# Kernel optimization log

Measured on AMD Instinct MI355X. Metric: run time of the kernel, lower is better.

Reference implementation:

```python
import jax, jax.numpy as jnp
import numpy as np

N_NODES = 100000
N_EDGES = 1600000
IN_CH = 50


def setup_inputs() -> dict:
    key = jax.random.key(0)
    ks = jax.random.split(key, 6)
    x = jax.random.normal(ks[0], (N_NODES, IN_CH), dtype=jnp.float32)
    edge_index = jax.random.randint(ks[1], (2, N_EDGES), 0, N_NODES, dtype=jnp.int32)
    # Glorot-ish scaled weights
    W1 = jax.random.normal(ks[2], (2 * IN_CH, 64), dtype=jnp.float32) * (1.0 / np.sqrt(2 * IN_CH))
    b1 = jnp.zeros((64,), jnp.float32)
    W2 = jax.random.normal(ks[3], (2 * 64, 32), dtype=jnp.float32) * (1.0 / np.sqrt(2 * 64))
    b2 = jnp.zeros((32,), jnp.float32)
    W3 = jax.random.normal(ks[4], (32, 1), dtype=jnp.float32) * (1.0 / np.sqrt(32))
    b3 = jnp.zeros((1,), jnp.float32)
    return {"x": x, "edge_index": edge_index, "W1": W1, "b1": b1,
            "W2": W2, "b2": b2, "W3": W3, "b3": b3}


def _sage_conv(x, src, dst, W, b, n_nodes):
    # mean aggregation of neighbor (source) features onto target nodes
    msg = x[src]                                             # [E, d] gather
    agg = jax.ops.segment_sum(msg, dst, num_segments=n_nodes)  # [N, d]
    cnt = jax.ops.segment_sum(jnp.ones(src.shape[0], x.dtype), dst,
                              num_segments=n_nodes)            # [N]
    mean = agg / jnp.maximum(cnt, 1.0)[:, None]
    h = jnp.concatenate([x, mean], axis=-1)                  # concat=True
    return h @ W + b


def reference(x, edge_index, W1, b1, W2, b2, W3, b3):
    src, dst = edge_index[0], edge_index[1]
    n = x.shape[0]
    h = jax.nn.relu(_sage_conv(x, src, dst, W1, b1, n))
    h = jax.nn.relu(_sage_conv(h, src, dst, W2, b2, n))
    return h @ W3 + b3  # [N, 1]
```

## Files before the change

kernel.cpp:

```cpp
#include <hip/hip_runtime.h>
#include <hip/hip_bf16.h>

#define N_NODES 100000
#define N_EDGES 1600000
#define IN_CH 50
#define NPB 256
#define NB ((N_NODES + NPB - 1) / NPB)
#define CAPLOG 13
#define EPB 4096
#define NBLK_A ((N_EDGES + EPB - 1) / EPB)
#define PAD_BLOCKS ((N_NODES * 64) / 1024)

__global__ __launch_bounds__(1024) void bin_pad_kernel(
    const int* __restrict__ src, const int* __restrict__ dst,
    int* __restrict__ cursor_rel, unsigned* __restrict__ binned,
    const float* __restrict__ x, unsigned short* __restrict__ xb) {
    if (blockIdx.x >= NBLK_A) {
        int t = (blockIdx.x - NBLK_A) * 1024 + threadIdx.x;
        int n = t >> 6, c = t & 63;
        float v = (c < IN_CH) ? x[n * IN_CH + c] : 0.0f;
        __hip_bfloat16 hb = __float2bfloat16(v);
        xb[t] = *(unsigned short*)&hb;
        return;
    }
    __shared__ int bc[NB];
    __shared__ int boff[NB];
    int t = threadIdx.x;
    if (t < NB) bc[t] = 0;
    __syncthreads();
    int e0 = blockIdx.x * EPB;
    int e1 = min(e0 + EPB, N_EDGES);
    for (int i = e0 + t; i < e1; i += 1024)
        atomicAdd(&bc[dst[i] >> 8], 1);
    __syncthreads();
    if (t < NB) {
        int v = bc[t];
        int rel = v ? atomicAdd(&cursor_rel[t], v) : 0;
        boff[t] = (t << CAPLOG) + rel;
        bc[t] = 0;
    }
    __syncthreads();
    for (int i = e0 + t; i < e1; i += 1024) {
        int d = dst[i];
        int b = d >> 8;
        int k = atomicAdd(&bc[b], 1);
        binned[boff[b] + k] = ((unsigned)(d & 255) << 17) | (unsigned)src[i];
    }
}

__global__ __launch_bounds__(1024) void bucket_fine(
    const unsigned* __restrict__ binned, const int* __restrict__ cursor_rel,
    int* __restrict__ cnt, int* __restrict__ row_start, int* __restrict__ csr_src) {
    __shared__ int lcnt[NPB];
    __shared__ int lofs[NPB];
    __shared__ int sc[NPB];
    int t = threadIdx.x;
    int b = blockIdx.x;
    int nbase = b * NPB;
    int bbase = b << CAPLOG;
    int ecnt  = cursor_rel[b];
    if (t < NPB) lcnt[t] = 0;
    __syncthreads();
    for (int i = t; i < ecnt; i += 1024)
        atomicAdd(&lcnt[(binned[bbase + i] >> 17) & 255], 1);
    __syncthreads();
    int v = (t < NPB) ? lcnt[t] : 0;
    if (t < NPB) sc[t] = v;
    __syncthreads();
    for (int off = 1; off < NPB; off <<= 1) {
        int tmp = (t < NPB && t >= off) ? sc[t - off] : 0;
        __syncthreads();
        if (t < NPB) sc[t] += tmp;
        __syncthreads();
    }
    if (t < NPB) {
        int excl = sc[t] - v;
        lofs[t] = excl;
        int n = nbase + t;
        if (n < N_NODES) { cnt[n] = v; row_start[n] = bbase + excl; }
    }
    __syncthreads();
    for (int i = t; i < ecnt; i += 1024) {
        unsigned p = binned[bbase + i];
        int d = (int)((p >> 17) & 255);
        int k = atomicAdd(&lofs[d], 1);
        csr_src[bbase + k] = (int)(p & 0x1FFFFu);
    }
}

__device__ __forceinline__ void upadd8(float* a, uint4 v, float p) {
    a[0] = fmaf(p, __uint_as_float(v.x << 16), a[0]);
    a[1] = fmaf(p, __uint_as_float(v.x & 0xffff0000u), a[1]);
    a[2] = fmaf(p, __uint_as_float(v.y << 16), a[2]);
    a[3] = fmaf(p, __uint_as_float(v.y & 0xffff0000u), a[3]);
    a[4] = fmaf(p, __uint_as_float(v.z << 16), a[4]);
    a[5] = fmaf(p, __uint_as_float(v.z & 0xffff0000u), a[5]);
    a[6] = fmaf(p, __uint_as_float(v.w << 16), a[6]);
    a[7] = fmaf(p, __uint_as_float(v.w & 0xffff0000u), a[7]);
}

#define WAVE_LDS_FENCE() __asm__ volatile("s_waitcnt lgkmcnt(0)" ::: "memory")

__device__ __forceinline__ void gather2(
    const unsigned short* __restrict__ featb, const int* __restrict__ csr_src,
    const int* __restrict__ row_start, const int* __restrict__ cnt,
    int nb, int lane, float acc[2][8]) {
    int g  = lane >> 3;
    int cw = (lane & 7) * 8;
    int start[2], deg[2], sv[2];
    #pragma unroll
    for (int i = 0; i < 2; ++i) {
        start[i] = row_start[nb + i];
        deg[i]   = cnt[nb + i];
        #pragma unroll
        for (int c = 0; c < 8; ++c) acc[i][c] = 0.f;
    }
    int dmax = max(deg[0], deg[1]);
    #pragma unroll
    for (int i = 0; i < 2; ++i)
        sv[i] = (lane < deg[i]) ? csr_src[start[i] + lane] : 0;

    #pragma unroll
    for (int cb = 0; cb < 64; cb += 16) {
        if (cb >= dmax) break;
        int s00 = __shfl(sv[0], cb + g);
        int s01 = __shfl(sv[0], cb + 8 + g);
        int s10 = __shfl(sv[1], cb + g);
        int s11 = __shfl(sv[1], cb + 8 + g);
        uint4 v00 = *(const uint4*)(featb + s00 * 64 + cw);
        uint4 v01 = *(const uint4*)(featb + s01 * 64 + cw);
        uint4 v10 = *(const uint4*)(featb + s10 * 64 + cw);
        uint4 v11 = *(const uint4*)(featb + s11 * 64 + cw);
        int rem0 = deg[0] - cb;
        int rem1 = deg[1] - cb;
        upadd8(acc[0], v00, (g < rem0) ? 1.f : 0.f);
        upadd8(acc[0], v01, (g + 8 < rem0) ? 1.f : 0.f);
        upadd8(acc[1], v10, (g < rem1) ? 1.f : 0.f);
        upadd8(acc[1], v11, (g + 8 < rem1) ? 1.f : 0.f);
    }
    if (dmax > 64) {
        for (int i = 0; i < 2; ++i) {
            for (int c0 = 64; c0 < deg[i]; c0 += 64) {
                int rem = deg[i] - c0; if (rem > 64) rem = 64;
                int sx = (lane < rem) ? csr_src[start[i] + c0 + lane] : 0;
                for (int cb = 0; cb < rem; cb += 16) {
                    int s0 = __shfl(sx, cb + g);
                    int s1 = __shfl(sx, cb + 8 + g);
                    float p0 = (cb + g < rem) ? 1.f : 0.f;
                    float p1 = (cb + 8 + g < rem) ? 1.f : 0.f;
                    uint4 v0 = *(const uint4*)(featb + s0 * 64 + cw);
                    uint4 v1 = *(const uint4*)(featb + s1 * 64 + cw);
                    upadd8(acc[i], v0, p0);
                    upadd8(acc[i], v1, p1);
                }
            }
        }
    }
    #pragma unroll
    for (int i = 0; i < 2; ++i) {
        float inv = 1.0f / fmaxf((float)deg[i], 1.0f);
        #pragma unroll
        for (int c = 0; c < 8; ++c) {
            float t = acc[i][c];
            t += __shfl_xor(t, 8);
            t += __shfl_xor(t, 16);
            t += __shfl_xor(t, 32);
            acc[i][c] = t * inv;
        }
    }
}

__device__ __forceinline__ float bf16u(unsigned short u) {
    return __uint_as_float(((unsigned)u) << 16);
}

__global__ __launch_bounds__(256, 8) void layer1_fused(
    const unsigned short* __restrict__ xb,
    const int* __restrict__ csr_src, const int* __restrict__ row_start,
    const int* __restrict__ cnt, const float* __restrict__ W1,
    const float* __restrict__ b1, unsigned short* __restrict__ h1b) {
    int wv   = threadIdx.x >> 6;
    int lane = threadIdx.x & 63;
    int nb   = (blockIdx.x * 4 + wv) * 2;

    float acc[2][8];
    gather2(xb, csr_src, row_start, cnt, nb, lane, acc);

    __shared__ __align__(16) float selfF[4][2][64];
    __shared__ __align__(16) float meanF[4][2][64];
    #pragma unroll
    for (int i = 0; i < 2; ++i) {
        selfF[wv][i][lane] = bf16u(xb[((nb + i) << 6) + lane]);
        if (lane < 8) {
            *(float4*)&meanF[wv][i][lane * 8] =
                make_float4(acc[i][0], acc[i][1], acc[i][2], acc[i][3]);
            *(float4*)&meanF[wv][i][lane * 8 + 4] =
                make_float4(acc[i][4], acc[i][5], acc[i][6], acc[i][7]);
        }
    }
    WAVE_LDS_FENCE();

    float ao[2];
    float bb = b1[lane];
    #pragma unroll
    for (int i = 0; i < 2; ++i) ao[i] = bb;
    #pragma unroll
    for (int k = 0; k < IN_CH; ++k) {
        float w = W1[k * 64 + lane];
        #pragma unroll
        for (int i = 0; i < 2; ++i) ao[i] = fmaf(selfF[wv][i][k], w, ao[i]);
    }
    #pragma unroll
    for (int k = 0; k < IN_CH; ++k) {
        float w = W1[(IN_CH + k) * 64 + lane];
        #pragma unroll
        for (int i = 0; i < 2; ++i) ao[i] = fmaf(meanF[wv][i][k], w, ao[i]);
    }
    #pragma unroll
    for (int i = 0; i < 2; ++i) {
        float r = fmaxf(ao[i], 0.f);
        __hip_bfloat16 hb = __float2bfloat16(r);
        h1b[((nb + i) << 6) + lane] = *(unsigned short*)&hb;
    }
}

__global__ __launch_bounds__(256, 8) void layer23_fused(
    const unsigned short* __restrict__ h1b,
    const int* __restrict__ csr_src, const int* __restrict__ row_start,
    const int* __restrict__ cnt, const float* __restrict__ W2,
    const float* __restrict__ b2, const float* __restrict__ W3,
    const float* __restrict__ b3, float* __restrict__ out) {
    int wv   = threadIdx.x >> 6;
    int lane = threadIdx.x & 63;
    int nb   = (blockIdx.x * 4 + wv) * 2;

    float acc[2][8];
    gather2(h1b, csr_src, row_start, cnt, nb, lane, acc);

    __shared__ __align__(16) float featL[4][2][128];
    #pragma unroll
    for (int i = 0; i < 2; ++i) {
        featL[wv][i][lane] = bf16u(h1b[((nb + i) << 6) + lane]);
        if (lane < 8) {
            *(float4*)&featL[wv][i][64 + lane * 8] =
                make_float4(acc[i][0], acc[i][1], acc[i][2], acc[i][3]);
            *(float4*)&featL[wv][i][64 + lane * 8 + 4] =
                make_float4(acc[i][4], acc[i][5], acc[i][6], acc[i][7]);
        }
    }
    WAVE_LDS_FENCE();

    int hh = lane >> 5;
    int j  = lane & 31;
    float a0 = b2[j];
    #pragma unroll
    for (int k = 0; k < 128; ++k) {
        float w = W2[k * 32 + j];
        a0 = fmaf(featL[wv][hh][k], w, a0);
    }
    float w3 = W3[j];
    float c3 = b3[0];
    float v0 = fmaxf(a0, 0.f) * w3;
    #pragma unroll
    for (int off = 1; off <= 16; off <<= 1)
        v0 += __shfl_xor(v0, off);
    if (j == 0)
        out[nb + hh] = v0 + c3;
}

extern "C" void kernel_launch(void* const* d_in, const int* in_sizes, int n_in,
                              void* d_out, int out_size, void* d_ws, size_t ws_size,
                              hipStream_t stream) {
    const float* x   = (const float*)d_in[0];
    const int*   ei  = (const int*)d_in[1];
    const int*   src = ei;
    const int*   dst = ei + N_EDGES;
    const float* W1  = (const float*)d_in[2];
    const float* b1  = (const float*)d_in[3];
    const float* W2  = (const float*)d_in[4];
    const float* b2  = (const float*)d_in[5];
    const float* W3  = (const float*)d_in[6];
    const float* b3  = (const float*)d_in[7];
    float* out = (float*)d_out;

    char* ws = (char*)d_ws;
    auto align = [](size_t v) { return (v + 255) & ~(size_t)255; };
    size_t o = 0;
    int* cursor_rel = (int*)(ws + o); o = align(o + 512 * 4);
    int* cnt       = (int*)(ws + o); o = align(o + (size_t)N_NODES * 4);
    int* row_start = (int*)(ws + o); o = align(o + (size_t)N_NODES * 4);
    unsigned* binned = (unsigned*)(ws + o); o = align(o + ((size_t)NB << CAPLOG) * 4);
    int* csr_src   = (int*)(ws + o); o = align(o + ((size_t)NB << CAPLOG) * 4);
    unsigned short* xb  = (unsigned short*)(ws + o); o = align(o + (size_t)N_NODES * 64 * 2);
    unsigned short* h1b = (unsigned short*)(ws + o); o = align(o + (size_t)N_NODES * 64 * 2);

    (void)hipMemsetAsync(cursor_rel, 0, 512 * sizeof(int), stream);

    bin_pad_kernel<<<NBLK_A + PAD_BLOCKS, 1024, 0, stream>>>(src, dst, cursor_rel,
                                                             binned, x, xb);
    bucket_fine<<<NB, 1024, 0, stream>>>(binned, cursor_rel, cnt, row_start, csr_src);

    layer1_fused<<<N_NODES / 8, 256, 0, stream>>>(xb, csr_src, row_start, cnt,
                                                  W1, b1, h1b);
    layer23_fused<<<N_NODES / 8, 256, 0, stream>>>(h1b, csr_src, row_start, cnt,
                                                   W2, b2, W3, b3, out);
}
```

Baseline: 249.6 us.

## Apply layer-2 weight before aggregation to halve gathered feature width

Because mean aggregation is linear, layer 1 now also multiplies h1 by both halves of W2, storing the self-projection in fp32 and the neighbor-projection in bf16 (32 channels). Layer 2 then gathers 32-wide bf16 rows instead of 64-wide, so the random-access edge gather moves half the bytes, and it only adds the two terms before ReLU and W3. The price is extra FMA work and a new fp32 intermediate in layer 1, plus a different bf16 rounding point for the aggregated values.

Result: slower. 418.9 us (+67.8%).

```diff
diff --git a/kernel.cpp b/kernel.cpp
--- a/kernel.cpp
+++ b/kernel.cpp
@@ -178,7 +178,9 @@
     const unsigned short* __restrict__ xb,
     const int* __restrict__ csr_src, const int* __restrict__ row_start,
     const int* __restrict__ cnt, const float* __restrict__ W1,
-    const float* __restrict__ b1, unsigned short* __restrict__ h1b) {
+    const float* __restrict__ b1, const float* __restrict__ W2,
+    const float* __restrict__ b2,
+    unsigned short* __restrict__ y2b, float* __restrict__ yselff) {
     int wv   = threadIdx.x >> 6;
     int lane = threadIdx.x & 63;
     int nb   = (blockIdx.x * 4 + wv) * 2;
@@ -216,35 +218,111 @@
         #pragma unroll
         for (int i = 0; i < 2; ++i) ao[i] = fmaf(meanF[wv][i][k], w, ao[i]);
     }
-    #pragma unroll
-    for (int i = 0; i < 2; ++i) {
-        float r = fmaxf(ao[i], 0.f);
-        __hip_bfloat16 hb = __float2bfloat16(r);
-        h1b[((nb + i) << 6) + lane] = *(unsigned short*)&hb;
-    }
+
+    __shared__ __align__(16) float h1F[4][2][64];
+    #pragma unroll
+    for (int i = 0; i < 2; ++i)
+        h1F[wv][i][lane] = fmaxf(ao[i], 0.f);
+    WAVE_LDS_FENCE();
+
+    int hh = lane >> 5;
+    int j  = lane & 31;
+    float ys = b2[j];
+    float ym = 0.f;
+    #pragma unroll
+    for (int k = 0; k < 64; ++k) {
+        float h = h1F[wv][hh][k];
+        ys = fmaf(h, W2[k * 32 + j], ys);
+        ym = fmaf(h, W2[(64 + k) * 32 + j], ym);
+    }
+    yselff[(nb + hh) * 32 + j] = ys;
+    __hip_bfloat16 hb = __float2bfloat16(ym);
+    y2b[(nb + hh) * 32 + j] = *(unsigned short*)&hb;
 }
 
 __global__ __launch_bounds__(256, 8) void layer23_fused(
-    const unsigned short* __restrict__ h1b,
+    const unsigned short* __restrict__ y2b,
     const int* __restrict__ csr_src, const int* __restrict__ row_start,
-    const int* __restrict__ cnt, const float* __restrict__ W2,
-    const float* __restrict__ b2, const float* __restrict__ W3,
-    const float* __restrict__ b3, float* __restrict__ out) {
+    const int* __restrict__ cnt, const float* __restrict__ yselff,
+    const float* __restrict__ W3, const float* __restrict__ b3,
+    float* __restrict__ out) {
     int wv   = threadIdx.x >> 6;
     int lane = threadIdx.x & 63;
     int nb   = (blockIdx.x * 4 + wv) * 2;
-
+    int g  = lane >> 2;
+    int cw = (lane & 3) * 8;
+
+    int start[2], deg[2], sv[2];
     float acc[2][8];
-    gather2(h1b, csr_src, row_start, cnt, nb, lane, acc);
-
-    __shared__ __align__(16) float featL[4][2][128];
-    #pragma unroll
-    for (int i = 0; i < 2; ++i) {
-        featL[wv][i][lane] = bf16u(h1b[((nb + i) << 6) + lane]);
-        if (lane < 8) {
-            *(float4*)&featL[wv][i][64 + lane * 8] =
+    #pragma unroll
+    for (int i = 0; i < 2; ++i) {
+        start[i] = row_start[nb + i];
+        deg[i]   = cnt[nb + i];
+        #pragma unroll
+        for (int c = 0; c < 8; ++c) acc[i][c] = 0.f;
+    }
+    int dmax = max(deg[0], deg[1]);
+    #pragma unroll
+    for (int i = 0; i < 2; ++i)
+        sv[i] = (lane < deg[i]) ? csr_src[start[i] + lane] : 0;
+
+    #pragma unroll
+    for (int cb = 0; cb < 64; cb += 32) {
+        if (cb >= dmax) break;
+        int s00 = __shfl(sv[0], cb + g);
+        int s01 = __shfl(sv[0], cb + 16 + g);
+        int s10 = __shfl(sv[1], cb + g);
+        int s11 = __shfl(sv[1], cb + 16 + g);
+        uint4 v00 = *(const uint4*)(y2b + s00 * 32 + cw);
+        uint4 v01 = *(const uint4*)(y2b + s01 * 32 + cw);
+        uint4 v10 = *(const uint4*)(y2b + s10 * 32 + cw);
+        uint4 v11 = *(const uint4*)(y2b + s11 * 32 + cw);
+        int rem0 = deg[0] - cb;
+        int rem1 = deg[1] - cb;
+        upadd8(acc[0], v00, (g < rem0) ? 1.f : 0.f);
+        upadd8(acc[0], v01, (g + 16 < rem0) ? 1.f : 0.f);
+        upadd8(acc[1], v10, (g < rem1) ? 1.f : 0.f);
+        upadd8(acc[1], v11, (g + 16 < rem1) ? 1.f : 0.f);
+    }
+    if (dmax > 64) {
+        for (int i = 0; i < 2; ++i) {
+            for (int c0 = 64; c0 < deg[i]; c0 += 64) {
+                int rem = deg[i] - c0; if (rem > 64) rem = 64;
+                int sx = (lane < rem) ? csr_src[start[i] + c0 + lane] : 0;
+                for (int cb = 0; cb < rem; cb += 32) {
+                    int s0 = __shfl(sx, cb + g);
+                    int s1 = __shfl(sx, cb + 16 + g);
+                    float p0 = (cb + g < rem) ? 1.f : 0.f;
+                    float p1 = (cb + 16 + g < rem) ? 1.f : 0.f;
+                    uint4 v0 = *(const uint4*)(y2b + s0 * 32 + cw);
+                    uint4 v1 = *(const uint4*)(y2b + s1 * 32 + cw);
+                    upadd8(acc[i], v0, p0);
+                    upadd8(acc[i], v1, p1);
+                }
+            }
+        }
+    }
+
+    __shared__ __align__(16) float aggF[4][2][32];
+    #pragma unroll
+    for (int i = 0; i < 2; ++i) {
+        float inv = 1.0f / fmaxf((float)deg[i], 1.0f);
+        #pragma unroll
+        for (int c = 0; c < 8; ++c) {
+            float t = acc[i][c];
+            t += __shfl_xor(t, 4);
+            t += __shfl_xor(t, 8);
+            t += __shfl_xor(t, 16);
+            t += __shfl_xor(t, 32);
+            acc[i][c] = t * inv;
+        }
+    }
+    if (lane < 4) {
+        #pragma unroll
+        for (int i = 0; i < 2; ++i) {
+            *(float4*)&aggF[wv][i][lane * 8] =
                 make_float4(acc[i][0], acc[i][1], acc[i][2], acc[i][3]);
-            *(float4*)&featL[wv][i][64 + lane * 8 + 4] =
+            *(float4*)&aggF[wv][i][lane * 8 + 4] =
                 make_float4(acc[i][4], acc[i][5], acc[i][6], acc[i][7]);
         }
     }
@@ -252,20 +330,13 @@
 
     int hh = lane >> 5;
     int j  = lane & 31;
-    float a0 = b2[j];
-    #pragma unroll
-    for (int k = 0; k < 128; ++k) {
-        float w = W2[k * 32 + j];
-        a0 = fmaf(featL[wv][hh][k], w, a0);
-    }
-    float w3 = W3[j];
-    float c3 = b3[0];
-    float v0 = fmaxf(a0, 0.f) * w3;
+    float pre = yselff[(nb + hh) * 32 + j] + aggF[wv][hh][j];
+    float v0 = fmaxf(pre, 0.f) * W3[j];
     #pragma unroll
     for (int off = 1; off <= 16; off <<= 1)
         v0 += __shfl_xor(v0, off);
     if (j == 0)
-        out[nb + hh] = v0 + c3;
+        out[nb + hh] = v0 + b3[0];
 }
 
 extern "C" void kernel_launch(void* const* d_in, const int* in_sizes, int n_in,
@@ -292,7 +363,8 @@
     unsigned* binned = (unsigned*)(ws + o); o = align(o + ((size_t)NB << CAPLOG) * 4);
     int* csr_src   = (int*)(ws + o); o = align(o + ((size_t)NB << CAPLOG) * 4);
     unsigned short* xb  = (unsigned short*)(ws + o); o = align(o + (size_t)N_NODES * 64 * 2);
-    unsigned short* h1b = (unsigned short*)(ws + o); o = align(o + (size_t)N_NODES * 64 * 2);
+    unsigned short* y2b = (unsigned short*)(ws + o); o = align(o + (size_t)N_NODES * 32 * 2);
+    float* yselff = (float*)(ws + o); o = align(o + (size_t)N_NODES * 32 * 4);
 
     (void)hipMemsetAsync(cursor_rel, 0, 512 * sizeof(int), stream);
 
@@ -301,7 +373,7 @@
     bucket_fine<<<NB, 1024, 0, stream>>>(binned, cursor_rel, cnt, row_start, csr_src);
 
     layer1_fused<<<N_NODES / 8, 256, 0, stream>>>(xb, csr_src, row_start, cnt,
-                                                  W1, b1, h1b);
-    layer23_fused<<<N_NODES / 8, 256, 0, stream>>>(h1b, csr_src, row_start, cnt,
-                                                   W2, b2, W3, b3, out);
-}
+                                                  W1, b1, W2, b2, y2b, yselff);
+    layer23_fused<<<N_NODES / 8, 256, 0, stream>>>(y2b, csr_src, row_start, cnt,
+                                                   yselff, W3, b3, out);
+}
```
